# Kernel optimization log

Hardware: AMD Instinct MI355X
Metric: run time of the kernel (lower is better)

Reference implementation:

```python
import jax, jax.numpy as jnp
import numpy as np
import math

B, L, C_IN = 32, 1024, 21
D_MODEL, N_HEADS, D_FF, E_LAYERS = 256, 8, 1024, 3
E = D_MODEL // N_HEADS
MOVING_AVG, FACTOR, NUM_CLASS = 5, 1.0, 3


def setup_inputs() -> dict:
    key = jax.random.key(0)
    ks = jax.random.split(key, 12)
    s = 0.05
    return {
        "x_enc": jax.random.normal(ks[0], (B, L, C_IN), jnp.float32),
        "token_w": jax.random.normal(ks[1], (D_MODEL, C_IN, 3), jnp.float32) * s,
        "qw": jax.random.normal(ks[2], (E_LAYERS, D_MODEL, D_MODEL), jnp.float32) * s,
        "qb": jnp.zeros((E_LAYERS, D_MODEL), jnp.float32),
        "kw": jax.random.normal(ks[3], (E_LAYERS, D_MODEL, D_MODEL), jnp.float32) * s,
        "kb": jnp.zeros((E_LAYERS, D_MODEL), jnp.float32),
        "vw": jax.random.normal(ks[4], (E_LAYERS, D_MODEL, D_MODEL), jnp.float32) * s,
        "vb": jnp.zeros((E_LAYERS, D_MODEL), jnp.float32),
        "ow": jax.random.normal(ks[5], (E_LAYERS, D_MODEL, D_MODEL), jnp.float32) * s,
        "ob": jnp.zeros((E_LAYERS, D_MODEL), jnp.float32),
        "c1w": jax.random.normal(ks[6], (E_LAYERS, D_FF, D_MODEL), jnp.float32) * s,
        "c2w": jax.random.normal(ks[7], (E_LAYERS, D_MODEL, D_FF), jnp.float32) * s,
        "norm_w": jnp.ones((D_MODEL,), jnp.float32),
        "norm_b": jnp.zeros((D_MODEL,), jnp.float32),
        "proj_w": jax.random.normal(ks[8], (NUM_CLASS, D_MODEL * L), jnp.float32) * 0.01,
        "proj_b": jnp.zeros((NUM_CLASS,), jnp.float32),
    }


def moving_mean(x, k):
    # x: (B, L, D); replicate-pad front/end by (k-1)//2 then average (AvgPool1d stride 1)
    p = (k - 1) // 2
    xp = jnp.concatenate([jnp.repeat(x[:, :1], p, 1), x, jnp.repeat(x[:, -1:], p, 1)], axis=1)
    Lx = x.shape[1]
    acc = xp[:, :Lx]
    for i in range(1, k):
        acc = acc + xp[:, i:i + Lx]
    return acc / k


def series_decomp(x, k):
    m = moving_mean(x, k)
    return x - m, m


def autocorrelation(q, k_, v):
    # q,k_,v: (B, L, H, E). Period-based dependency via FFT cross-correlation.
    Lq = q.shape[1]
    qf = jnp.fft.rfft(q.transpose(0, 2, 3, 1), axis=-1)   # (B,H,E,L//2+1)
    kf = jnp.fft.rfft(k_.transpose(0, 2, 3, 1), axis=-1)
    corr = jnp.fft.irfft(qf * jnp.conj(kf), n=Lq, axis=-1)  # (B,H,E,L)
    vals = v.transpose(0, 2, 3, 1)                          # (B,H,E,L)
    top_k = int(FACTOR * math.log(Lq))
    mean_corr = corr.mean(axis=(1, 2))                      # (B,L)
    weights, delay = jax.lax.top_k(mean_corr, top_k)        # (B,k)
    w = jax.nn.softmax(weights, axis=-1)                    # (B,k)
    # rolled gather: pattern[b,h,e,i,l] = vals[b,h,e,(l+delay[b,i]) % L]
    idx = (jnp.arange(Lq)[None, None, :] + delay[:, :, None]) % Lq  # (B,k,L)
    patterns = jax.vmap(lambda vb, ib: vb[:, :, ib])(vals, idx)      # (B,H,E,k,L)
    out = jnp.einsum('bhekl,bk->bhel', patterns, w)
    return out.transpose(0, 3, 1, 2)  # (B,L,H,E)


def encoder_layer(x, qw, qb, kw, kb, vw, vb, ow, ob, c1w, c2w):
    Bx, Lx, _ = x.shape
    q = (x @ qw.T + qb).reshape(Bx, Lx, N_HEADS, E)
    k_ = (x @ kw.T + kb).reshape(Bx, Lx, N_HEADS, E)
    v = (x @ vw.T + vb).reshape(Bx, Lx, N_HEADS, E)
    a = autocorrelation(q, k_, v).reshape(Bx, Lx, D_MODEL)
    a = a @ ow.T + ob
    x, _ = series_decomp(x + a, MOVING_AVG)
    y = jax.nn.gelu(jnp.einsum('bld,fd->blf', x, c1w), approximate=False)  # Conv1d k=1
    y = jnp.einsum('blf,df->bld', y, c2w)
    res, _ = series_decomp(x + y, MOVING_AVG)
    return res


def my_layernorm(x, w, b):
    mu = x.mean(-1, keepdims=True)
    var = ((x - mu) ** 2).mean(-1, keepdims=True)
    xh = (x - mu) / jnp.sqrt(var + 1e-5) * w + b
    return xh - xh.mean(axis=1, keepdims=True)  # subtract seasonal bias over time


def token_embed(x, w):
    # circular-padded Conv1d(C_IN -> D_MODEL, kernel 3, no bias)
    xt = x.transpose(0, 2, 1)                                   # (B,C,L)
    xp = jnp.pad(xt, ((0, 0), (0, 0), (1, 1)), mode='wrap')
    out = jax.lax.conv_general_dilated(xp, w, (1,), 'VALID')     # (B,D,L)
    return out.transpose(0, 2, 1)


def reference(x_enc, token_w, qw, qb, kw, kb, vw, vb, ow, ob, c1w, c2w, norm_w, norm_b, proj_w, proj_b):
    x = token_embed(x_enc, token_w)
    for l in range(E_LAYERS):
        x = encoder_layer(x, qw[l], qb[l], kw[l], kb[l], vw[l], vb[l], ow[l], ob[l], c1w[l], c2w[l])
    x = my_layernorm(x, norm_w, norm_b)
    out = jax.nn.gelu(x, approximate=False)
    out = out.reshape(out.shape[0], -1)  # (B, L*D_MODEL)
    return out @ proj_w.T + proj_b
```

## Files before the change

kernel.cpp:

```cpp
#include <hip/hip_runtime.h>
#include <hip/hip_bf16.h>
#include <math.h>

#define BB 32
#define LL 1024
#define C_IN 21
#define DM 256
#define DFF 1024
#define NLAYERS 3
#define TOPK 6
#define TOPC 16
#define LSCALE 4096.0f
#define LINV (1.0f/4096.0f)

typedef __attribute__((ext_vector_type(8))) short short8v;
typedef __attribute__((ext_vector_type(8))) _Float16 half8;
typedef __attribute__((ext_vector_type(4))) float f32x4;

__device__ __forceinline__ float gelu_f(float v){
    return 0.5f * v * (1.0f + erff(v * 0.7071067811865476f));
}
__device__ __forceinline__ ushort f2h_bits(float f){
    _Float16 h = (_Float16)f;
    return __builtin_bit_cast(ushort, h);
}
__device__ __forceinline__ float h2f(ushort u){
    return (float)__builtin_bit_cast(_Float16, u);
}

__global__ __launch_bounds__(256) void split_w_k(const float* __restrict__ src,
                                                 ushort* __restrict__ h, ushort* __restrict__ l, int n){
    int i = blockIdx.x*256 + threadIdx.x;
    if (i < n){
        float f = src[i];
        _Float16 hh = (_Float16)f;
        h[i] = __builtin_bit_cast(ushort, hh);
        l[i] = f2h_bits((f - (float)hh) * LSCALE);
    }
}
__global__ __launch_bounds__(256) void split_w_strided(const float* __restrict__ src,
                                                       ushort* __restrict__ h, ushort* __restrict__ l,
                                                       int n, int src_ls, int dst_ls, int dst_off){
    int i = blockIdx.x*256 + threadIdx.x;
    if (i < n){
        int layer = i / src_ls, r = i % src_ls;
        float f = src[i];
        _Float16 hh = (_Float16)f;
        size_t d = (size_t)layer*dst_ls + dst_off + r;
        h[d] = __builtin_bit_cast(ushort, hh);
        l[d] = f2h_bits((f - (float)hh) * LSCALE);
    }
}
__global__ __launch_bounds__(256) void cat_bias_k(const float* __restrict__ b1,
                                                  const float* __restrict__ b2,
                                                  float* __restrict__ out, int n){
    int i = blockIdx.x*256 + threadIdx.x;
    if (i < n){
        int layer = i / 512, c = i % 512;
        out[i] = (c < 256) ? b1[layer*256 + c] : b2[layer*256 + c - 256];
    }
}
__global__ __launch_bounds__(256) void transpose_tw(const float* __restrict__ src,
                                                    float* __restrict__ dst){
    int i = blockIdx.x*256 + threadIdx.x;
    if (i < 256*63){
        int d = i / 63, k = i % 63;
        dst[k*256 + d] = src[i];
    }
}

__global__ __launch_bounds__(256) void token_embed_k(const float* __restrict__ x,
                                                     const float* __restrict__ wT,
                                                     float* __restrict__ out){
    int b = blockIdx.x, l0 = blockIdx.y*32;
    int d = threadIdx.x;
    __shared__ float xs[34][C_IN];
    for (int i = threadIdx.x; i < 34*C_IN; i += 256){
        int r = i / C_IN, c = i % C_IN;
        int g = (l0 - 1 + r + LL) & (LL-1);
        xs[r][c] = x[(size_t)b*LL*C_IN + (size_t)g*C_IN + c];
    }
    float w[63];
    #pragma unroll
    for (int k=0;k<63;k++) w[k] = wT[k*256 + d];
    __syncthreads();
    for (int i=0;i<32;i++){
        float acc = 0.f;
        #pragma unroll
        for (int c=0;c<C_IN;c++){
            acc += xs[i][c]   * w[c*3+0];
            acc += xs[i+1][c] * w[c*3+1];
            acc += xs[i+2][c] * w[c*3+2];
        }
        out[((size_t)b*LL + l0+i)*DM + d] = acc;
    }
}

template<int AMODE, bool BIAS, bool GELU, int OMODE, bool ZSPLIT>
__global__ __launch_bounds__(256) void gemm_mfma_split(const void* __restrict__ Av,
                                                       const void* __restrict__ Av2,
                                                       const ushort* __restrict__ Wh,
                                                       const ushort* __restrict__ Wl,
                                                       const float* __restrict__ bias,
                                                       void* __restrict__ Cv,
                                                       void* __restrict__ C2v,
                                                       void* __restrict__ C3v,
                                                       void* __restrict__ C4v,
                                                       int M, int N, int K){
    __shared__ __align__(16) ushort Ah_s[128*32];
    __shared__ __align__(16) ushort Al_s[128*32];
    __shared__ __align__(16) ushort Wh_s[64*32];
    __shared__ __align__(16) ushort Wl_s[64*32];

    const int tid = threadIdx.x;
    const int MB = M >> 7;
    const int bx = blockIdx.x % MB, by = blockIdx.x / MB;
    const int bm = bx << 7, bn = by << 6;

    const int lane = tid & 63;
    const int wid  = tid >> 6;
    const int wm = wid >> 1, wn = wid & 1;
    const int lr = lane & 15, lg = lane >> 4;

    int aoff[4], boff[2];
    #pragma unroll
    for (int f=0; f<4; f++){
        int ar = wm*64 + f*16 + lr;
        aoff[f] = ar*32 + (lg ^ ((ar>>1)&3))*8;
    }
    #pragma unroll
    for (int g=0; g<2; g++){
        int br = wn*32 + g*16 + lr;
        boff[g] = br*32 + (lg ^ ((br>>1)&3))*8;
    }

    f32x4 acc[4][2], accX[4][2];
    #pragma unroll
    for (int i=0;i<4;i++)
        #pragma unroll
        for (int j=0;j<2;j++){
            acc[i][j]  = (f32x4){0.f,0.f,0.f,0.f};
            accX[i][j] = (f32x4){0.f,0.f,0.f,0.f};
        }

    const int kbeg = ZSPLIT ? (int)blockIdx.y * (K>>1) : 0;
    const int kend = ZSPLIT ? kbeg + (K>>1) : K;

    for (int k0=kbeg; k0<kend; k0+=32){
        #pragma unroll
        for (int i=0;i<2;i++){
            int c = i*256 + tid;
            int row = c >> 2, ko = c & 3;
            int sw = ko ^ ((row>>1)&3);
            int dst = row*32 + sw*8;
            if (AMODE == 2){
                const ushort* Ah_g = (const ushort*)Av;
                const ushort* Al_g = (const ushort*)Av2;
                size_t src = (size_t)(bm+row)*K + k0 + ko*8;
                *reinterpret_cast<short8v*>(&Ah_s[dst]) = *reinterpret_cast<const short8v*>(Ah_g + src);
                *reinterpret_cast<short8v*>(&Al_s[dst]) = *reinterpret_cast<const short8v*>(Al_g + src);
            } else {
                const float* A = (const float*)Av;
                const float* p = A + (size_t)(bm+row)*K + k0 + ko*8;
                float4 f0 = *reinterpret_cast<const float4*>(p);
                float4 f1 = *reinterpret_cast<const float4*>(p+4);
                float vals[8] = {f0.x,f0.y,f0.z,f0.w,f1.x,f1.y,f1.z,f1.w};
                short8v hv, lv;
                #pragma unroll
                for (int j=0;j<8;j++){
                    _Float16 hh = (_Float16)vals[j];
                    hv[j] = (short)__builtin_bit_cast(ushort, hh);
                    lv[j] = (short)f2h_bits((vals[j] - (float)hh) * LSCALE);
                }
                *reinterpret_cast<short8v*>(&Ah_s[dst]) = hv;
                *reinterpret_cast<short8v*>(&Al_s[dst]) = lv;
            }
        }
        {
            int row = tid >> 2, ko = tid & 3;
            int sw = ko ^ ((row>>1)&3);
            int dst = row*32 + sw*8;
            size_t src = (size_t)(bn+row)*K + k0 + ko*8;
            *reinterpret_cast<short8v*>(&Wh_s[dst]) = *reinterpret_cast<const short8v*>(Wh + src);
            *reinterpret_cast<short8v*>(&Wl_s[dst]) = *reinterpret_cast<const short8v*>(Wl + src);
        }
        __syncthreads();

        short8v af[4], al[4], bf_[2], bl[2];
        #pragma unroll
        for (int f=0; f<4; f++){
            af[f] = *reinterpret_cast<short8v*>(&Ah_s[aoff[f]]);
            al[f] = *reinterpret_cast<short8v*>(&Al_s[aoff[f]]);
        }
        #pragma unroll
        for (int g=0; g<2; g++){
            bf_[g] = *reinterpret_cast<short8v*>(&Wh_s[boff[g]]);
            bl[g]  = *reinterpret_cast<short8v*>(&Wl_s[boff[g]]);
        }
        #pragma unroll
        for (int i=0;i<4;i++){
            #pragma unroll
            for (int j=0;j<2;j++){
                acc[i][j] = __builtin_amdgcn_mfma_f32_16x16x32_f16(
                    __builtin_bit_cast(half8, af[i]), __builtin_bit_cast(half8, bf_[j]), acc[i][j], 0,0,0);
                accX[i][j] = __builtin_amdgcn_mfma_f32_16x16x32_f16(
                    __builtin_bit_cast(half8, af[i]), __builtin_bit_cast(half8, bl[j]), accX[i][j], 0,0,0);
                accX[i][j] = __builtin_amdgcn_mfma_f32_16x16x32_f16(
                    __builtin_bit_cast(half8, al[i]), __builtin_bit_cast(half8, bf_[j]), accX[i][j], 0,0,0);
            }
        }
        __syncthreads();
    }

    float* Cout0 = (float*)((ZSPLIT && blockIdx.y) ? C2v : Cv);
    const int crow0 = bm + wm*64, ccol0 = bn + wn*32;
    #pragma unroll
    for (int i=0;i<4;i++){
        #pragma unroll
        for (int j=0;j<2;j++){
            int row0 = crow0 + i*16 + lg*4;
            int col  = ccol0 + j*16 + lr;
            float bv = (BIAS && (!ZSPLIT || blockIdx.y==0)) ? bias[col] : 0.f;
            #pragma unroll
            for (int r=0;r<4;r++){
                float v = acc[i][j][r] + accX[i][j][r]*LINV + bv;
                if (GELU) v = gelu_f(v);
                if (OMODE == 0){
                    Cout0[(size_t)(row0+r)*N + col] = v;
                } else if (OMODE == 2){
                    size_t idx = (size_t)(row0+r)*N + col;
                    _Float16 hh = (_Float16)v;
                    ((ushort*)Cv)[idx]  = __builtin_bit_cast(ushort, hh);
                    ((ushort*)C2v)[idx] = f2h_bits((v - (float)hh) * LSCALE);
                } else {
                    _Float16 hh = (_Float16)v;
                    ushort hb = __builtin_bit_cast(ushort, hh);
                    ushort lb = f2h_bits((v - (float)hh) * LSCALE);
                    if (col < 256){
                        size_t idx = (size_t)(row0+r)*256 + col;
                        ((ushort*)Cv)[idx]  = hb;
                        ((ushort*)C2v)[idx] = lb;
                    } else {
                        size_t idx = (size_t)(row0+r)*256 + (col-256);
                        ((ushort*)C3v)[idx] = hb;
                        ((ushort*)C4v)[idx] = lb;
                    }
                }
            }
        }
    }
}

__global__ __launch_bounds__(256) void corr_mfma(const ushort* __restrict__ qh,
                                                 const ushort* __restrict__ kh,
                                                 float* __restrict__ scr){
    __shared__ __align__(16) ushort Qh_s[128*32];
    __shared__ __align__(16) ushort Kh_s[128*32];
    __shared__ float bins[255];

    const int tid = threadIdx.x;
    int flat = blockIdx.x;
    flat = (flat & 7) * 256 + (flat >> 3);
    const int bxt = flat & 7;
    const int byt = (flat >> 3) & 7;
    const int b   = flat >> 6;
    const int bi = bxt * 128, bj = byt * 128;

    for (int i=tid; i<255; i+=256) bins[i] = 0.f;

    const int lane = tid & 63;
    const int wid  = tid >> 6;
    const int wm = wid >> 1, wn = wid & 1;
    const int lr = lane & 15, lg = lane >> 4;

    int aoff[4], boff[4];
    #pragma unroll
    for (int f=0; f<4; f++){
        int ar = wm*64 + f*16 + lr;
        aoff[f] = ar*32 + (lg ^ ((ar>>1)&3))*8;
        int br = wn*64 + f*16 + lr;
        boff[f] = br*32 + (lg ^ ((br>>1)&3))*8;
    }

    f32x4 acc[4][4];
    #pragma unroll
    for (int i=0;i<4;i++)
        #pragma unroll
        for (int j=0;j<4;j++)
            acc[i][j] = (f32x4){0.f,0.f,0.f,0.f};

    const size_t qbase = (size_t)b*LL*DM;

    for (int k0=0; k0<DM; k0+=32){
        #pragma unroll
        for (int i=0;i<2;i++){
            int c = i*256 + tid;
            int row = c >> 2, ko = c & 3;
            int sw = ko ^ ((row>>1)&3);
            int dst = row*32 + sw*8;
            *reinterpret_cast<short8v*>(&Qh_s[dst]) =
                *reinterpret_cast<const short8v*>(qh + qbase + (size_t)(bi+row)*DM + k0 + ko*8);
            *reinterpret_cast<short8v*>(&Kh_s[dst]) =
                *reinterpret_cast<const short8v*>(kh + qbase + (size_t)(bj+row)*DM + k0 + ko*8);
        }
        __syncthreads();

        short8v ah[4], bh4[4];
        #pragma unroll
        for (int f=0; f<4; f++){
            ah[f]  = *reinterpret_cast<short8v*>(&Qh_s[aoff[f]]);
            bh4[f] = *reinterpret_cast<short8v*>(&Kh_s[boff[f]]);
        }
        #pragma unroll
        for (int i=0;i<4;i++)
            #pragma unroll
            for (int j=0;j<4;j++)
                acc[i][j] = __builtin_amdgcn_mfma_f32_16x16x32_f16(
                    __builtin_bit_cast(half8, ah[i]), __builtin_bit_cast(half8, bh4[j]), acc[i][j], 0,0,0);
        __syncthreads();
    }

    float pre[7][4];
    #pragma unroll
    for (int d=0; d<7; d++)
        #pragma unroll
        for (int r=0;r<4;r++) pre[d][r]=0.f;
    #pragma unroll
    for (int i=0;i<4;i++)
        #pragma unroll
        for (int j=0;j<4;j++)
            #pragma unroll
            for (int r=0;r<4;r++)
                pre[i-j+3][r] += acc[i][j][r];
    const int bbase = wm*64 - wn*64 + lg*4 - lr + 127;
    #pragma unroll
    for (int d=0; d<7; d++)
        #pragma unroll
        for (int r=0;r<4;r++)
            atomicAdd(&bins[bbase + 16*(d-3) + r], pre[d][r]);
    __syncthreads();
    float* slot = scr + ((size_t)(b*64 + byt*8 + bxt) << 8);
    for (int i=tid; i<255; i+=256) slot[i] = bins[i];
}

__global__ __launch_bounds__(256) void corr_reduce(const float* __restrict__ scr,
                                                   float* __restrict__ mc){
    int b = blockIdx.x;
    int t = blockIdx.y*256 + threadIdx.x;
    float s = 0.f;
    const float* base = scr + ((size_t)b << 14);
    #pragma unroll
    for (int byt=0; byt<8; byt++){
        #pragma unroll
        for (int bxt=0; bxt<8; bxt++){
            int i = (t - 128*(bxt - byt) + 127) & (LL-1);
            if (i < 255) s += base[((byt*8 + bxt) << 8) + i];
        }
    }
    mc[(size_t)b*LL + t] = s * (1.f/256.f);
}

__global__ __launch_bounds__(256) void topcand_kernel(const float* __restrict__ mc,
                                                      int* __restrict__ cand){
    int b = blockIdx.x, tid = threadIdx.x;
    __shared__ float sv[LL];
    __shared__ float rv[256];
    __shared__ int ri[256];
    for (int i=tid;i<LL;i+=256) sv[i] = mc[(size_t)b*LL + i];
    __syncthreads();
    for (int it=0; it<TOPC; it++){
        float best = -1e30f; int bi = LL;
        for (int i=tid;i<LL;i+=256){
            float v = sv[i];
            if (v > best || (v == best && i < bi)){ best = v; bi = i; }
        }
        rv[tid]=best; ri[tid]=bi;
        __syncthreads();
        for (int s=128;s>0;s>>=1){
            if (tid < s){
                if (rv[tid+s] > rv[tid] || (rv[tid+s]==rv[tid] && ri[tid+s]<ri[tid])){
                    rv[tid]=rv[tid+s]; ri[tid]=ri[tid+s];
                }
            }
            __syncthreads();
        }
        if (tid==0){ cand[b*TOPC+it]=ri[0]; sv[ri[0]] = -1e30f; }
        __syncthreads();
    }
}

__global__ __launch_bounds__(256) void rescore_k(const ushort* __restrict__ qh,
                                                 const ushort* __restrict__ ql,
                                                 const ushort* __restrict__ kh,
                                                 const ushort* __restrict__ kl,
                                                 const int* __restrict__ cand,
                                                 float* __restrict__ scores4){
    int i = blockIdx.x;
    int b = (i & 7) | (((i >> 3) & 3) << 3);
    int c = i >> 5;
    int chunk = blockIdx.y;
    int t = cand[b*TOPC + c];
    const size_t base = (size_t)b << 18;
    const int off = t << 8;
    const int mbeg = chunk << 16;
    const int mend = mbeg + (1<<16);
    float s = 0.f, comp = 0.f;
    for (int m = mbeg + threadIdx.x*8; m < mend; m += 256*8){
        int mq = (m + off) & ((1<<18)-1);
        short8v kh8 = *reinterpret_cast<const short8v*>(kh + base + m);
        short8v kl8 = *reinterpret_cast<const short8v*>(kl + base + m);
        short8v qh8 = *reinterpret_cast<const short8v*>(qh + base + mq);
        short8v ql8 = *reinterpret_cast<const short8v*>(ql + base + mq);
        float term = 0.f;
        #pragma unroll
        for (int j=0;j<8;j++){
            float kf = h2f((ushort)kh8[j]) + h2f((ushort)kl8[j])*LINV;
            float qf = h2f((ushort)qh8[j]) + h2f((ushort)ql8[j])*LINV;
            term += kf*qf;
        }
        float y = term - comp;
        float tt = s + y;
        comp = (tt - s) - y;
        s = tt;
    }
    for (int o=32;o>0;o>>=1) s += __shfl_down(s, o, 64);
    __shared__ float red[4];
    if ((threadIdx.x & 63)==0) red[threadIdx.x>>6] = s;
    __syncthreads();
    if (threadIdx.x==0)
        scores4[(size_t)(b*TOPC + c)*4 + chunk] = red[0]+red[1]+red[2]+red[3];
}

__global__ __launch_bounds__(64) void finalize_k(const int* __restrict__ cand,
                                                 const float* __restrict__ scores4,
                                                 int* __restrict__ delays,
                                                 float* __restrict__ wts){
    int b = blockIdx.x;
    int lane = threadIdx.x;
    float v = -1e30f;
    int idx = 1<<30;
    if (lane < TOPC){
        size_t s4 = (size_t)(b*TOPC + lane)*4;
        v = (scores4[s4] + scores4[s4+1] + scores4[s4+2] + scores4[s4+3]) * (1.f/256.f);
        idx = cand[b*TOPC + lane];
    }
    float topv[TOPK]; int topi[TOPK];
    #pragma unroll
    for (int k=0;k<TOPK;k++){
        float bv = v; int bi = idx;
        #pragma unroll
        for (int o=8;o>0;o>>=1){
            float ov = __shfl_xor(bv, o, 16);
            int   oi = __shfl_xor(bi, o, 16);
            if (ov > bv || (ov == bv && oi < bi)){ bv = ov; bi = oi; }
        }
        topv[k]=bv; topi[k]=bi;
        if (idx == bi) v = -1e30f;
    }
    if (lane==0){
        float mx = topv[0];
        float e[TOPK], se=0.f;
        #pragma unroll
        for (int k=0;k<TOPK;k++){ e[k]=expf(topv[k]-mx); se+=e[k]; }
        #pragma unroll
        for (int k=0;k<TOPK;k++){
            wts[b*TOPK+k] = e[k]/se;
            delays[b*TOPK+k] = topi[k];
        }
    }
}

__global__ __launch_bounds__(256) void attn_gather4(const float4* __restrict__ v,
                                                    const int* __restrict__ delays,
                                                    const float* __restrict__ wts,
                                                    float4* __restrict__ a){
    int gid = blockIdx.x*256 + threadIdx.x;
    int d4 = gid & 63;
    int bl = gid >> 6;
    int b = bl >> 10, l = bl & (LL-1);
    const int* dl = delays + b*TOPK;
    const float* w = wts + b*TOPK;
    float ax=0.f, ay=0.f, az=0.f, aw=0.f;
    #pragma unroll
    for (int kk=0;kk<TOPK;kk++){
        int ls = (l + dl[kk]) & (LL-1);
        float4 t = v[(size_t)((b<<10)+ls)*64 + d4];
        float wk = w[kk];
        ax += wk*t.x; ay += wk*t.y; az += wk*t.z; aw += wk*t.w;
    }
    a[gid] = make_float4(ax, ay, az, aw);
}

__global__ __launch_bounds__(256) void add_decomp4(const float4* __restrict__ xa,
                                                   const float4* __restrict__ xb,
                                                   float4* __restrict__ out){
    int d4 = threadIdx.x & 63;
    int rg = threadIdx.x >> 6;
    int b = blockIdx.x;
    int l0 = blockIdx.y*128 + rg*32;
    float4 win[5];
    #pragma unroll
    for (int i=0;i<4;i++){
        int g = l0 - 2 + i;
        g = g < 0 ? 0 : g;
        size_t idx = (size_t)((b<<10) + g)*64 + d4;
        float4 A = xa[idx], Bv = xb[idx];
        win[i] = make_float4(A.x+Bv.x, A.y+Bv.y, A.z+Bv.z, A.w+Bv.w);
    }
    for (int i=0;i<32;i++){
        int g = l0 + 2 + i;
        g = g > LL-1 ? LL-1 : g;
        size_t idx = (size_t)((b<<10) + g)*64 + d4;
        float4 A = xa[idx], Bv = xb[idx];
        win[4] = make_float4(A.x+Bv.x, A.y+Bv.y, A.z+Bv.z, A.w+Bv.w);
        float4 o;
        o.x = win[2].x - (win[0].x+win[1].x+win[2].x+win[3].x+win[4].x)*0.2f;
        o.y = win[2].y - (win[0].y+win[1].y+win[2].y+win[3].y+win[4].y)*0.2f;
        o.z = win[2].z - (win[0].z+win[1].z+win[2].z+win[3].z+win[4].z)*0.2f;
        o.w = win[2].w - (win[0].w+win[1].w+win[2].w+win[3].w+win[4].w)*0.2f;
        out[(size_t)((b<<10) + l0 + i)*64 + d4] = o;
        win[0]=win[1]; win[1]=win[2]; win[2]=win[3]; win[3]=win[4];
    }
}

__global__ __launch_bounds__(256) void add_decomp4_3(const float4* __restrict__ xa,
                                                     const float4* __restrict__ xb,
                                                     const float4* __restrict__ xc,
                                                     float4* __restrict__ out){
    int d4 = threadIdx.x & 63;
    int rg = threadIdx.x >> 6;
    int b = blockIdx.x;
    int l0 = blockIdx.y*128 + rg*32;
    float4 win[5];
    #pragma unroll
    for (int i=0;i<4;i++){
        int g = l0 - 2 + i;
        g = g < 0 ? 0 : g;
        size_t idx = (size_t)((b<<10) + g)*64 + d4;
        float4 A = xa[idx], Bv = xb[idx], Cc = xc[idx];
        win[i] = make_float4(A.x+Bv.x+Cc.x, A.y+Bv.y+Cc.y, A.z+Bv.z+Cc.z, A.w+Bv.w+Cc.w);
    }
    for (int i=0;i<32;i++){
        int g = l0 + 2 + i;
        g = g > LL-1 ? LL-1 : g;
        size_t idx = (size_t)((b<<10) + g)*64 + d4;
        float4 A = xa[idx], Bv = xb[idx], Cc = xc[idx];
        win[4] = make_float4(A.x+Bv.x+Cc.x, A.y+Bv.y+Cc.y, A.z+Bv.z+Cc.z, A.w+Bv.w+Cc.w);
        float4 o;
        o.x = win[2].x - (win[0].x+win[1].x+win[2].x+win[3].x+win[4].x)*0.2f;
        o.y = win[2].y - (win[0].y+win[1].y+win[2].y+win[3].y+win[4].y)*0.2f;
        o.z = win[2].z - (win[0].z+win[1].z+win[2].z+win[3].z+win[4].z)*0.2f;
        o.w = win[2].w - (win[0].w+win[1].w+win[2].w+win[3].w+win[4].w)*0.2f;
        out[(size_t)((b<<10) + l0 + i)*64 + d4] = o;
        win[0]=win[1]; win[1]=win[2]; win[2]=win[3]; win[3]=win[4];
    }
}

__global__ __launch_bounds__(256) void ln_kernel(const float* __restrict__ x,
                                                 const float* __restrict__ nw,
                                                 const float* __restrict__ nb,
                                                 float* __restrict__ xh){
    int bl = blockIdx.x, d = threadIdx.x;
    float val = x[(size_t)bl*DM + d];
    __shared__ float red[4];
    float v = val;
    for (int o=32;o>0;o>>=1) v += __shfl_down(v, o, 64);
    if ((d&63)==0) red[d>>6] = v;
    __syncthreads();
    float mu = (red[0]+red[1]+red[2]+red[3])*(1.f/256.f);
    __syncthreads();
    float diff = val - mu;
    v = diff*diff;
    for (int o=32;o>0;o>>=1) v += __shfl_down(v, o, 64);
    if ((d&63)==0) red[d>>6] = v;
    __syncthreads();
    float var = (red[0]+red[1]+red[2]+red[3])*(1.f/256.f);
    xh[(size_t)bl*DM + d] = diff*rsqrtf(var+1e-5f)*nw[d] + nb[d];
}

__global__ __launch_bounds__(256) void colsum_kernel(const float* __restrict__ xh,
                                                     float* __restrict__ colsum){
    int b = blockIdx.x, chunk = blockIdx.y, d = threadIdx.x;
    float s = 0.f;
    for (int l = chunk*128; l < (chunk+1)*128; l++)
        s += xh[((size_t)b*LL + l)*DM + d];
    atomicAdd(&colsum[b*DM + d], s);
}

__global__ __launch_bounds__(256) void gelu_sub_kernel(const float* __restrict__ xh,
                                                       const float* __restrict__ colsum,
                                                       float* __restrict__ g){
    int bl = blockIdx.x, d = threadIdx.x;
    int b = bl / LL;
    float v = xh[(size_t)bl*DM + d] - colsum[b*DM + d]*(1.f/1024.f);
    g[(size_t)bl*DM + d] = gelu_f(v);
}

__global__ __launch_bounds__(256) void proj_kernel(const float* __restrict__ g,
                                                   const float* __restrict__ pw,
                                                   const float* __restrict__ pb,
                                                   float* __restrict__ out){
    int b = blockIdx.x, c = blockIdx.y, ch = blockIdx.z;
    int tid = threadIdx.x;
    const size_t F = (size_t)LL*DM;
    size_t base = ch*(F/16);
    float s = 0.f;
    for (size_t i = tid; i < F/16; i += 256)
        s += g[(size_t)b*F + base + i] * pw[(size_t)c*F + base + i];
    for (int o=32;o>0;o>>=1) s += __shfl_down(s, o, 64);
    __shared__ float red[4];
    if ((tid&63)==0) red[tid>>6] = s;
    __syncthreads();
    if (tid==0){
        float tot = red[0]+red[1]+red[2]+red[3];
        if (ch==0) tot += pb[c];
        atomicAdd(&out[b*3 + c], tot);
    }
}

extern "C" void kernel_launch(void* const* d_in, const int* in_sizes, int n_in,
                              void* d_out, int out_size, void* d_ws, size_t ws_size,
                              hipStream_t stream) {
    const float* x_enc   = (const float*)d_in[0];
    const float* token_w = (const float*)d_in[1];
    const float* qw = (const float*)d_in[2];
    const float* qb = (const float*)d_in[3];
    const float* kw = (const float*)d_in[4];
    const float* kb = (const float*)d_in[5];
    const float* vw = (const float*)d_in[6];
    const float* vb = (const float*)d_in[7];
    const float* ow = (const float*)d_in[8];
    const float* ob = (const float*)d_in[9];
    const float* c1w = (const float*)d_in[10];
    const float* c2w = (const float*)d_in[11];
    const float* norm_w = (const float*)d_in[12];
    const float* norm_b = (const float*)d_in[13];
    const float* proj_w = (const float*)d_in[14];
    const float* proj_b = (const float*)d_in[15];
    float* outp = (float*)d_out;

    const size_t NTOK = (size_t)BB*LL*DM;
    float* ws = (float*)d_ws;
    float* buf0 = ws;
    float* buf1 = ws + NTOK;
    float* buf2 = ws + 2*NTOK;
    ushort* wu = (ushort*)(ws + 3*NTOK);
    const size_t WSM = (size_t)NLAYERS*DM*DM;
    const size_t WSF = (size_t)NLAYERS*DFF*DM;
    ushort* qkwh = wu;             ushort* qkwl = qkwh + 2*WSM;
    ushort* vwh  = qkwl + 2*WSM;   ushort* vwl  = vwh + WSM;
    ushort* owh  = vwl + WSM;      ushort* owl  = owh + WSM;
    ushort* c1wh = owl + WSM;      ushort* c1wl = c1wh + WSF;
    ushort* c2wh = c1wl + WSF;     ushort* c2wl = c2wh + WSF;
    float* after_w = ws + 3*NTOK + 2359296;
    float* qkbias = after_w;
    float* mc     = qkbias + (size_t)NLAYERS*512;
    float* colsum = mc + (size_t)BB*LL;
    int*   delays = (int*)(colsum + BB*DM);
    float* wts    = (float*)(delays + BB*TOPK);
    int*   cand   = (int*)(wts + BB*TOPK);
    float* scores4 = (float*)(cand + BB*TOPC);
    float* twT    = scores4 + BB*TOPC*4;
    float* scr    = twT + 63*256;
    float* buf3   = scr + 524288;

    const size_t needed_floats = 3*NTOK + 2359296 + (size_t)NLAYERS*512 + (size_t)BB*LL
                               + (size_t)BB*DM + (size_t)BB*TOPK*2 + (size_t)BB*TOPC
                               + (size_t)BB*TOPC*4 + 63*256 + 524288 + NTOK;
    const bool zs = (ws_size >= needed_floats*sizeof(float));

    hipMemsetAsync(d_out, 0, 96*sizeof(float), stream);

    {
        int n1 = NLAYERS*DM*DM;
        int n2 = NLAYERS*DFF*DM;
        split_w_strided<<<(n1+255)/256, 256, 0, stream>>>(qw, qkwh, qkwl, n1, 65536, 131072, 0);
        split_w_strided<<<(n1+255)/256, 256, 0, stream>>>(kw, qkwh, qkwl, n1, 65536, 131072, 65536);
        cat_bias_k<<<(NLAYERS*512+255)/256, 256, 0, stream>>>(qb, kb, qkbias, NLAYERS*512);
        split_w_k<<<(n1+255)/256, 256, 0, stream>>>(vw, vwh, vwl, n1);
        split_w_k<<<(n1+255)/256, 256, 0, stream>>>(ow, owh, owl, n1);
        split_w_k<<<(n2+255)/256, 256, 0, stream>>>(c1w, c1wh, c1wl, n2);
        split_w_k<<<(n2+255)/256, 256, 0, stream>>>(c2w, c2wh, c2wl, n2);
        transpose_tw<<<(256*63+255)/256, 256, 0, stream>>>(token_w, twT);
    }

    token_embed_k<<<dim3(BB, LL/32), 256, 0, stream>>>(x_enc, twT, buf0);

    const int M = BB*LL;
    const int FFNC = 8192;

    for (int l=0; l<NLAYERS; l++){
        ushort* qkwh_l = qkwh + (size_t)l*512*DM;  ushort* qkwl_l = qkwl + (size_t)l*512*DM;
        ushort* vwh_l = vwh + (size_t)l*DM*DM;     ushort* vwl_l = vwl + (size_t)l*DM*DM;
        ushort* owh_l = owh + (size_t)l*DM*DM;     ushort* owl_l = owl + (size_t)l*DM*DM;
        ushort* c1wh_l = c1wh + (size_t)l*DFF*DM;  ushort* c1wl_l = c1wl + (size_t)l*DFF*DM;
        ushort* c2wh_l = c2wh + (size_t)l*DM*DFF;  ushort* c2wl_l = c2wl + (size_t)l*DM*DFF;
        const float* qkb_l = qkbias + (size_t)l*512;
        const float* vb_l = vb + (size_t)l*DM;
        const float* ob_l = ob + (size_t)l*DM;

        ushort* qh_p = (ushort*)buf1;  ushort* ql_p = qh_p + NTOK;
        ushort* kh_p = (ushort*)buf2;  ushort* kl_p = kh_p + NTOK;
        gemm_mfma_split<0,true,false,3,false><<<(M/128)*(512/64), 256, 0, stream>>>(
            buf0, nullptr, qkwh_l, qkwl_l, qkb_l, qh_p, ql_p, kh_p, kl_p, M, 512, DM);

        corr_mfma<<<2048, 256, 0, stream>>>(qh_p, kh_p, scr);
        corr_reduce<<<dim3(BB, 4), 256, 0, stream>>>(scr, mc);
        topcand_kernel<<<BB, 256, 0, stream>>>(mc, cand);
        rescore_k<<<dim3(BB*TOPC, 4), 256, 0, stream>>>(qh_p, ql_p, kh_p, kl_p, cand, scores4);
        finalize_k<<<BB, 64, 0, stream>>>(cand, scores4, delays, wts);

        gemm_mfma_split<0,true,false,0,false><<<(M/128)*(DM/64), 256, 0, stream>>>(
            buf0, nullptr, vwh_l, vwl_l, vb_l, buf1, nullptr, nullptr, nullptr, M, DM, DM);
        attn_gather4<<<(BB*LL*64)/256, 256, 0, stream>>>(
            (const float4*)buf1, delays, wts, (float4*)buf2);
        gemm_mfma_split<0,true,false,0,false><<<(M/128)*(DM/64), 256, 0, stream>>>(
            buf2, nullptr, owh_l, owl_l, ob_l, buf1, nullptr, nullptr, nullptr, M, DM, DM);

        add_decomp4<<<dim3(BB, LL/128), 256, 0, stream>>>(
            (const float4*)buf0, (const float4*)buf1, (float4*)buf2);

        ushort* yh_p = (ushort*)buf0;
        ushort* yl_p = yh_p + (size_t)FFNC*DFF;
        for (int c0 = 0; c0 < M; c0 += FFNC){
            gemm_mfma_split<0,false,true,2,false><<<(FFNC/128)*(DFF/64), 256, 0, stream>>>(
                buf2 + (size_t)c0*DM, nullptr, c1wh_l, c1wl_l, nullptr, yh_p, yl_p, nullptr, nullptr, FFNC, DFF, DM);
            if (zs){
                gemm_mfma_split<2,false,false,0,true><<<dim3((FFNC/128)*(DM/64), 2), 256, 0, stream>>>(
                    yh_p, yl_p, c2wh_l, c2wl_l, nullptr,
                    buf1 + (size_t)c0*DM, buf3 + (size_t)c0*DM, nullptr, nullptr, FFNC, DM, DFF);
            } else {
                gemm_mfma_split<2,false,false,0,false><<<(FFNC/128)*(DM/64), 256, 0, stream>>>(
                    yh_p, yl_p, c2wh_l, c2wl_l, nullptr,
                    buf1 + (size_t)c0*DM, nullptr, nullptr, nullptr, FFNC, DM, DFF);
            }
        }

        if (zs)
            add_decomp4_3<<<dim3(BB, LL/128), 256, 0, stream>>>(
                (const float4*)buf2, (const float4*)buf1, (const float4*)buf3, (float4*)buf0);
        else
            add_decomp4<<<dim3(BB, LL/128), 256, 0, stream>>>(
                (const float4*)buf2, (const float4*)buf1, (float4*)buf0);
    }

    ln_kernel<<<BB*LL, 256, 0, stream>>>(buf0, norm_w, norm_b, buf1);
    hipMemsetAsync(colsum, 0, (size_t)BB*DM*sizeof(float), stream);
    colsum_kernel<<<dim3(BB, 8), 256, 0, stream>>>(buf1, colsum);
    gelu_sub_kernel<<<BB*LL, 256, 0, stream>>>(buf1, colsum, buf2);
    proj_kernel<<<dim3(BB, 3, 16), 256, 0, stream>>>(buf2, proj_w, proj_b, outp);
}
```

Measured before the change: 1.840 ms.

## Store activations as pre-split fp16 hi/lo pairs instead of fp32

Producers of GEMM inputs (token embedding, attention gather, decomposition kernels) now write activations directly as fp16 high plus scaled fp16 low halves, and all GEMMs read these split pairs. This removes the per-tile fp32-to-split conversion inside the GEMM loaders and the AMODE template path, and the activation bytes are the same (two 2-byte halves instead of one 4-byte float). Buffers are reassigned across the layer to fit the new layout. Elementwise kernels pay extra conversion work, and reconstruction via hi+lo*2^-12 may slightly change precision.

Result: no change. 1.828 ms (-0.6%).

```diff
diff --git a/kernel.cpp b/kernel.cpp
--- a/kernel.cpp
+++ b/kernel.cpp
@@ -26,6 +26,22 @@
 }
 __device__ __forceinline__ float h2f(ushort u){
     return (float)__builtin_bit_cast(_Float16, u);
+}
+__device__ __forceinline__ float4 loadp4(const ushort* __restrict__ h, const ushort* __restrict__ l, size_t i4){
+    ushort4 hv = *reinterpret_cast<const ushort4*>(h + 4*i4);
+    ushort4 lv = *reinterpret_cast<const ushort4*>(l + 4*i4);
+    return make_float4(h2f(hv.x)+h2f(lv.x)*LINV, h2f(hv.y)+h2f(lv.y)*LINV,
+                       h2f(hv.z)+h2f(lv.z)*LINV, h2f(hv.w)+h2f(lv.w)*LINV);
+}
+__device__ __forceinline__ void storep4(ushort* __restrict__ h, ushort* __restrict__ l, size_t i4, float4 v){
+    ushort4 hv, lv;
+    _Float16 a;
+    a=(_Float16)v.x; hv.x=__builtin_bit_cast(ushort,a); lv.x=f2h_bits((v.x-(float)a)*LSCALE);
+    a=(_Float16)v.y; hv.y=__builtin_bit_cast(ushort,a); lv.y=f2h_bits((v.y-(float)a)*LSCALE);
+    a=(_Float16)v.z; hv.z=__builtin_bit_cast(ushort,a); lv.z=f2h_bits((v.z-(float)a)*LSCALE);
+    a=(_Float16)v.w; hv.w=__builtin_bit_cast(ushort,a); lv.w=f2h_bits((v.w-(float)a)*LSCALE);
+    *reinterpret_cast<ushort4*>(h + 4*i4) = hv;
+    *reinterpret_cast<ushort4*>(l + 4*i4) = lv;
 }
 
 __global__ __launch_bounds__(256) void split_w_k(const float* __restrict__ src,
@@ -71,7 +87,8 @@
 
 __global__ __launch_bounds__(256) void token_embed_k(const float* __restrict__ x,
                                                      const float* __restrict__ wT,
-                                                     float* __restrict__ out){
+                                                     ushort* __restrict__ oh,
+                                                     ushort* __restrict__ ol){
     int b = blockIdx.x, l0 = blockIdx.y*32;
     int d = threadIdx.x;
     __shared__ float xs[34][C_IN];
@@ -92,13 +109,16 @@
             acc += xs[i+1][c] * w[c*3+1];
             acc += xs[i+2][c] * w[c*3+2];
         }
-        out[((size_t)b*LL + l0+i)*DM + d] = acc;
-    }
-}
-
-template<int AMODE, bool BIAS, bool GELU, int OMODE, bool ZSPLIT>
-__global__ __launch_bounds__(256) void gemm_mfma_split(const void* __restrict__ Av,
-                                                       const void* __restrict__ Av2,
+        size_t idx = ((size_t)b*LL + l0+i)*DM + d;
+        _Float16 hh = (_Float16)acc;
+        oh[idx] = __builtin_bit_cast(ushort, hh);
+        ol[idx] = f2h_bits((acc - (float)hh) * LSCALE);
+    }
+}
+
+template<bool BIAS, bool GELU, int OMODE, bool ZSPLIT>
+__global__ __launch_bounds__(256) void gemm_mfma_split(const ushort* __restrict__ Ah_g,
+                                                       const ushort* __restrict__ Al_g,
                                                        const ushort* __restrict__ Wh,
                                                        const ushort* __restrict__ Wl,
                                                        const float* __restrict__ bias,
@@ -153,28 +173,9 @@
             int row = c >> 2, ko = c & 3;
             int sw = ko ^ ((row>>1)&3);
             int dst = row*32 + sw*8;
-            if (AMODE == 2){
-                const ushort* Ah_g = (const ushort*)Av;
-                const ushort* Al_g = (const ushort*)Av2;
-                size_t src = (size_t)(bm+row)*K + k0 + ko*8;
-                *reinterpret_cast<short8v*>(&Ah_s[dst]) = *reinterpret_cast<const short8v*>(Ah_g + src);
-                *reinterpret_cast<short8v*>(&Al_s[dst]) = *reinterpret_cast<const short8v*>(Al_g + src);
-            } else {
-                const float* A = (const float*)Av;
-                const float* p = A + (size_t)(bm+row)*K + k0 + ko*8;
-                float4 f0 = *reinterpret_cast<const float4*>(p);
-                float4 f1 = *reinterpret_cast<const float4*>(p+4);
-                float vals[8] = {f0.x,f0.y,f0.z,f0.w,f1.x,f1.y,f1.z,f1.w};
-                short8v hv, lv;
-                #pragma unroll
-                for (int j=0;j<8;j++){
-                    _Float16 hh = (_Float16)vals[j];
-                    hv[j] = (short)__builtin_bit_cast(ushort, hh);
-                    lv[j] = (short)f2h_bits((vals[j] - (float)hh) * LSCALE);
-                }
-                *reinterpret_cast<short8v*>(&Ah_s[dst]) = hv;
-                *reinterpret_cast<short8v*>(&Al_s[dst]) = lv;
-            }
+            size_t src = (size_t)(bm+row)*K + k0 + ko*8;
+            *reinterpret_cast<short8v*>(&Ah_s[dst]) = *reinterpret_cast<const short8v*>(Ah_g + src);
+            *reinterpret_cast<short8v*>(&Al_s[dst]) = *reinterpret_cast<const short8v*>(Al_g + src);
         }
         {
             int row = tid >> 2, ko = tid & 3;
@@ -473,7 +474,8 @@
 __global__ __launch_bounds__(256) void attn_gather4(const float4* __restrict__ v,
                                                     const int* __restrict__ delays,
                                                     const float* __restrict__ wts,
-                                                    float4* __restrict__ a){
+                                                    ushort* __restrict__ ah,
+                                                    ushort* __restrict__ al){
     int gid = blockIdx.x*256 + threadIdx.x;
     int d4 = gid & 63;
     int bl = gid >> 6;
@@ -488,12 +490,14 @@
         float wk = w[kk];
         ax += wk*t.x; ay += wk*t.y; az += wk*t.z; aw += wk*t.w;
     }
-    a[gid] = make_float4(ax, ay, az, aw);
-}
-
-__global__ __launch_bounds__(256) void add_decomp4(const float4* __restrict__ xa,
-                                                   const float4* __restrict__ xb,
-                                                   float4* __restrict__ out){
+    storep4(ah, al, gid, make_float4(ax, ay, az, aw));
+}
+
+__global__ __launch_bounds__(256) void add_decomp_pf_p(const ushort* __restrict__ xah,
+                                                       const ushort* __restrict__ xal,
+                                                       const float4* __restrict__ xb,
+                                                       ushort* __restrict__ oh,
+                                                       ushort* __restrict__ ol){
     int d4 = threadIdx.x & 63;
     int rg = threadIdx.x >> 6;
     int b = blockIdx.x;
@@ -504,29 +508,31 @@
         int g = l0 - 2 + i;
         g = g < 0 ? 0 : g;
         size_t idx = (size_t)((b<<10) + g)*64 + d4;
-        float4 A = xa[idx], Bv = xb[idx];
+        float4 A = loadp4(xah, xal, idx), Bv = xb[idx];
         win[i] = make_float4(A.x+Bv.x, A.y+Bv.y, A.z+Bv.z, A.w+Bv.w);
     }
     for (int i=0;i<32;i++){
         int g = l0 + 2 + i;
         g = g > LL-1 ? LL-1 : g;
         size_t idx = (size_t)((b<<10) + g)*64 + d4;
-        float4 A = xa[idx], Bv = xb[idx];
+        float4 A = loadp4(xah, xal, idx), Bv = xb[idx];
         win[4] = make_float4(A.x+Bv.x, A.y+Bv.y, A.z+Bv.z, A.w+Bv.w);
         float4 o;
         o.x = win[2].x - (win[0].x+win[1].x+win[2].x+win[3].x+win[4].x)*0.2f;
         o.y = win[2].y - (win[0].y+win[1].y+win[2].y+win[3].y+win[4].y)*0.2f;
         o.z = win[2].z - (win[0].z+win[1].z+win[2].z+win[3].z+win[4].z)*0.2f;
         o.w = win[2].w - (win[0].w+win[1].w+win[2].w+win[3].w+win[4].w)*0.2f;
-        out[(size_t)((b<<10) + l0 + i)*64 + d4] = o;
+        storep4(oh, ol, (size_t)((b<<10) + l0 + i)*64 + d4, o);
         win[0]=win[1]; win[1]=win[2]; win[2]=win[3]; win[3]=win[4];
     }
 }
 
-__global__ __launch_bounds__(256) void add_decomp4_3(const float4* __restrict__ xa,
-                                                     const float4* __restrict__ xb,
-                                                     const float4* __restrict__ xc,
-                                                     float4* __restrict__ out){
+__global__ __launch_bounds__(256) void add_decomp3_pff_p(const ushort* __restrict__ xah,
+                                                         const ushort* __restrict__ xal,
+                                                         const float4* __restrict__ xb,
+                                                         const float4* __restrict__ xc,
+                                                         ushort* __restrict__ oh,
+                                                         ushort* __restrict__ ol){
     int d4 = threadIdx.x & 63;
     int rg = threadIdx.x >> 6;
     int b = blockIdx.x;
@@ -537,31 +543,33 @@
         int g = l0 - 2 + i;
         g = g < 0 ? 0 : g;
         size_t idx = (size_t)((b<<10) + g)*64 + d4;
-        float4 A = xa[idx], Bv = xb[idx], Cc = xc[idx];
+        float4 A = loadp4(xah, xal, idx), Bv = xb[idx], Cc = xc[idx];
         win[i] = make_float4(A.x+Bv.x+Cc.x, A.y+Bv.y+Cc.y, A.z+Bv.z+Cc.z, A.w+Bv.w+Cc.w);
     }
     for (int i=0;i<32;i++){
         int g = l0 + 2 + i;
         g = g > LL-1 ? LL-1 : g;
         size_t idx = (size_t)((b<<10) + g)*64 + d4;
-        float4 A = xa[idx], Bv = xb[idx], Cc = xc[idx];
+        float4 A = loadp4(xah, xal, idx), Bv = xb[idx], Cc = xc[idx];
         win[4] = make_float4(A.x+Bv.x+Cc.x, A.y+Bv.y+Cc.y, A.z+Bv.z+Cc.z, A.w+Bv.w+Cc.w);
         float4 o;
         o.x = win[2].x - (win[0].x+win[1].x+win[2].x+win[3].x+win[4].x)*0.2f;
         o.y = win[2].y - (win[0].y+win[1].y+win[2].y+win[3].y+win[4].y)*0.2f;
         o.z = win[2].z - (win[0].z+win[1].z+win[2].z+win[3].z+win[4].z)*0.2f;
         o.w = win[2].w - (win[0].w+win[1].w+win[2].w+win[3].w+win[4].w)*0.2f;
-        out[(size_t)((b<<10) + l0 + i)*64 + d4] = o;
+        storep4(oh, ol, (size_t)((b<<10) + l0 + i)*64 + d4, o);
         win[0]=win[1]; win[1]=win[2]; win[2]=win[3]; win[3]=win[4];
     }
 }
 
-__global__ __launch_bounds__(256) void ln_kernel(const float* __restrict__ x,
+__global__ __launch_bounds__(256) void ln_kernel(const ushort* __restrict__ xh_,
+                                                 const ushort* __restrict__ xl_,
                                                  const float* __restrict__ nw,
                                                  const float* __restrict__ nb,
                                                  float* __restrict__ xh){
     int bl = blockIdx.x, d = threadIdx.x;
-    float val = x[(size_t)bl*DM + d];
+    size_t i = (size_t)bl*DM + d;
+    float val = h2f(xh_[i]) + h2f(xl_[i])*LINV;
     __shared__ float red[4];
     float v = val;
     for (int o=32;o>0;o>>=1) v += __shfl_down(v, o, 64);
@@ -575,7 +583,7 @@
     if ((d&63)==0) red[d>>6] = v;
     __syncthreads();
     float var = (red[0]+red[1]+red[2]+red[3])*(1.f/256.f);
-    xh[(size_t)bl*DM + d] = diff*rsqrtf(var+1e-5f)*nw[d] + nb[d];
+    xh[i] = diff*rsqrtf(var+1e-5f)*nw[d] + nb[d];
 }
 
 __global__ __launch_bounds__(256) void colsum_kernel(const float* __restrict__ xh,
@@ -684,7 +692,8 @@
         transpose_tw<<<(256*63+255)/256, 256, 0, stream>>>(token_w, twT);
     }
 
-    token_embed_k<<<dim3(BB, LL/32), 256, 0, stream>>>(x_enc, twT, buf0);
+    ushort* xh_p = (ushort*)buf0;  ushort* xl_p = xh_p + NTOK;
+    token_embed_k<<<dim3(BB, LL/32), 256, 0, stream>>>(x_enc, twT, xh_p, xl_p);
 
     const int M = BB*LL;
     const int FFNC = 8192;
@@ -701,8 +710,8 @@
 
         ushort* qh_p = (ushort*)buf1;  ushort* ql_p = qh_p + NTOK;
         ushort* kh_p = (ushort*)buf2;  ushort* kl_p = kh_p + NTOK;
-        gemm_mfma_split<0,true,false,3,false><<<(M/128)*(512/64), 256, 0, stream>>>(
-            buf0, nullptr, qkwh_l, qkwl_l, qkb_l, qh_p, ql_p, kh_p, kl_p, M, 512, DM);
+        gemm_mfma_split<true,false,3,false><<<(M/128)*(512/64), 256, 0, stream>>>(
+            xh_p, xl_p, qkwh_l, qkwl_l, qkb_l, qh_p, ql_p, kh_p, kl_p, M, 512, DM);
 
         corr_mfma<<<2048, 256, 0, stream>>>(qh_p, kh_p, scr);
         corr_reduce<<<dim3(BB, 4), 256, 0, stream>>>(scr, mc);
@@ -710,41 +719,44 @@
         rescore_k<<<dim3(BB*TOPC, 4), 256, 0, stream>>>(qh_p, ql_p, kh_p, kl_p, cand, scores4);
         finalize_k<<<BB, 64, 0, stream>>>(cand, scores4, delays, wts);
 
-        gemm_mfma_split<0,true,false,0,false><<<(M/128)*(DM/64), 256, 0, stream>>>(
-            buf0, nullptr, vwh_l, vwl_l, vb_l, buf1, nullptr, nullptr, nullptr, M, DM, DM);
+        gemm_mfma_split<true,false,0,false><<<(M/128)*(DM/64), 256, 0, stream>>>(
+            xh_p, xl_p, vwh_l, vwl_l, vb_l, buf3, nullptr, nullptr, nullptr, M, DM, DM);
+        ushort* ah_p = (ushort*)buf1;  ushort* al_p = ah_p + NTOK;
         attn_gather4<<<(BB*LL*64)/256, 256, 0, stream>>>(
-            (const float4*)buf1, delays, wts, (float4*)buf2);
-        gemm_mfma_split<0,true,false,0,false><<<(M/128)*(DM/64), 256, 0, stream>>>(
-            buf2, nullptr, owh_l, owl_l, ob_l, buf1, nullptr, nullptr, nullptr, M, DM, DM);
-
-        add_decomp4<<<dim3(BB, LL/128), 256, 0, stream>>>(
-            (const float4*)buf0, (const float4*)buf1, (float4*)buf2);
+            (const float4*)buf3, delays, wts, ah_p, al_p);
+        gemm_mfma_split<true,false,0,false><<<(M/128)*(DM/64), 256, 0, stream>>>(
+            ah_p, al_p, owh_l, owl_l, ob_l, buf2, nullptr, nullptr, nullptr, M, DM, DM);
+
+        ushort* x1h_p = (ushort*)buf1;  ushort* x1l_p = x1h_p + NTOK;
+        add_decomp_pf_p<<<dim3(BB, LL/128), 256, 0, stream>>>(
+            xh_p, xl_p, (const float4*)buf2, x1h_p, x1l_p);
 
         ushort* yh_p = (ushort*)buf0;
         ushort* yl_p = yh_p + (size_t)FFNC*DFF;
         for (int c0 = 0; c0 < M; c0 += FFNC){
-            gemm_mfma_split<0,false,true,2,false><<<(FFNC/128)*(DFF/64), 256, 0, stream>>>(
-                buf2 + (size_t)c0*DM, nullptr, c1wh_l, c1wl_l, nullptr, yh_p, yl_p, nullptr, nullptr, FFNC, DFF, DM);
+            gemm_mfma_split<false,true,2,false><<<(FFNC/128)*(DFF/64), 256, 0, stream>>>(
+                x1h_p + (size_t)c0*DM, x1l_p + (size_t)c0*DM, c1wh_l, c1wl_l, nullptr,
+                yh_p, yl_p, nullptr, nullptr, FFNC, DFF, DM);
             if (zs){
-                gemm_mfma_split<2,false,false,0,true><<<dim3((FFNC/128)*(DM/64), 2), 256, 0, stream>>>(
+                gemm_mfma_split<false,false,0,true><<<dim3((FFNC/128)*(DM/64), 2), 256, 0, stream>>>(
                     yh_p, yl_p, c2wh_l, c2wl_l, nullptr,
-                    buf1 + (size_t)c0*DM, buf3 + (size_t)c0*DM, nullptr, nullptr, FFNC, DM, DFF);
+                    buf2 + (size_t)c0*DM, buf3 + (size_t)c0*DM, nullptr, nullptr, FFNC, DM, DFF);
             } else {
-                gemm_mfma_split<2,false,false,0,false><<<(FFNC/128)*(DM/64), 256, 0, stream>>>(
+                gemm_mfma_split<false,false,0,false><<<(FFNC/128)*(DM/64), 256, 0, stream>>>(
                     yh_p, yl_p, c2wh_l, c2wl_l, nullptr,
-                    buf1 + (size_t)c0*DM, nullptr, nullptr, nullptr, FFNC, DM, DFF);
+                    buf2 + (size_t)c0*DM, nullptr, nullptr, nullptr, FFNC, DM, DFF);
             }
         }
 
         if (zs)
-            add_decomp4_3<<<dim3(BB, LL/128), 256, 0, stream>>>(
-                (const float4*)buf2, (const float4*)buf1, (const float4*)buf3, (float4*)buf0);
+            add_decomp3_pff_p<<<dim3(BB, LL/128), 256, 0, stream>>>(
+                x1h_p, x1l_p, (const float4*)buf2, (const float4*)buf3, xh_p, xl_p);
         else
-            add_decomp4<<<dim3(BB, LL/128), 256, 0, stream>>>(
-                (const float4*)buf2, (const float4*)buf1, (float4*)buf0);
-    }
-
-    ln_kernel<<<BB*LL, 256, 0, stream>>>(buf0, norm_w, norm_b, buf1);
+            add_decomp_pf_p<<<dim3(BB, LL/128), 256, 0, stream>>>(
+                x1h_p, x1l_p, (const float4*)buf2, xh_p, xl_p);
+    }
+
+    ln_kernel<<<BB*LL, 256, 0, stream>>>(xh_p, xl_p, norm_w, norm_b, buf1);
     hipMemsetAsync(colsum, 0, (size_t)BB*DM*sizeof(float), stream);
     colsum_kernel<<<dim3(BB, 8), 256, 0, stream>>>(buf1, colsum);
     gelu_sub_kernel<<<BB*LL, 256, 0, stream>>>(buf1, colsum, buf2);
```
